# Kernel optimization log

Hardware: AMD Instinct MI355X
Metric: run time of the kernel (lower is better)

## Reference

```python
import jax, jax.numpy as jnp
import numpy as np
from jax import lax

HEAD = 8; DIM = 16; R = 3; R_T = 2
K_AREA = (2 * R + 1) ** 2   # 49 window positions
NT = 2 * R_T + 1            # 5 time taps
POSENC_SCALE = 10; N_FREQ = 10  # enc_dims=64 -> 64//(2*3)=10 freqs per axis


def conv3d(x, w, b):
    y = lax.conv_general_dilated(x, w, (1, 1, 1), 'SAME',
                                 dimension_numbers=('NCDHW', 'OIDHW', 'NCDHW'))
    return y + b[None, :, None, None, None]


def make_coord2(h, w):
    # LIIF-style pixel-center coords in [-1,1], channel order (y, x)
    ys = -1.0 + (2.0 * jnp.arange(h) + 1.0) / h
    xs = -1.0 + (2.0 * jnp.arange(w) + 1.0) / w
    yy, xx = jnp.meshgrid(ys, xs, indexing='ij')
    return jnp.stack([yy, xx], -1)


def gather2d_nearest(img, coord_yx):
    # img (B,C,H,W); coord (B,Q,K,2) normalized (y,x); grid_sample nearest, align_corners=False, zero pad
    B, C, H, W = img.shape
    iy = jnp.round(((coord_yx[..., 0] + 1.0) * H - 1.0) / 2.0)
    ix = jnp.round(((coord_yx[..., 1] + 1.0) * W - 1.0) / 2.0)
    valid = (iy >= 0) & (iy < H) & (ix >= 0) & (ix < W)
    idx = (jnp.clip(iy, 0, H - 1) * W + jnp.clip(ix, 0, W - 1)).astype(jnp.int32)
    flat = idx.reshape(B, -1)
    out = jnp.take_along_axis(img.reshape(B, C, H * W), flat[:, None, :], axis=2)
    out = out.reshape(B, C, *idx.shape[1:]) * valid[:, None].astype(img.dtype)
    return out  # (B,C,Q,K)


def trilinear(vol, coord_tyx):
    # vol (B,C,D,H,W); coord (B,Q,3) normalized (t,y,x); grid_sample bilinear 3D, align_corners=False, zero pad
    B, C, D, H, W = vol.shape
    iz = ((coord_tyx[..., 0] + 1.0) * D - 1.0) / 2.0
    iy = ((coord_tyx[..., 1] + 1.0) * H - 1.0) / 2.0
    ix = ((coord_tyx[..., 2] + 1.0) * W - 1.0) / 2.0
    z0 = jnp.floor(iz); y0 = jnp.floor(iy); x0 = jnp.floor(ix)
    wz = iz - z0; wy = iy - y0; wx = ix - x0
    volf = vol.reshape(B, C, D * H * W)

    def corner(zc, yc, xc, w):
        valid = (zc >= 0) & (zc < D) & (yc >= 0) & (yc < H) & (xc >= 0) & (xc < W)
        idx = (jnp.clip(zc, 0, D - 1) * (H * W) + jnp.clip(yc, 0, H - 1) * W
               + jnp.clip(xc, 0, W - 1)).astype(jnp.int32)
        v = jnp.take_along_axis(volf, idx[:, None, :], axis=2)  # (B,C,Q)
        return v * (w * valid.astype(vol.dtype))[:, None, :]

    out = 0.0
    for dz in (0, 1):
        for dy in (0, 1):
            for dx in (0, 1):
                w = ((wz if dz else 1 - wz) * (wy if dy else 1 - wy)
                     * (wx if dx else 1 - wx))
                out = out + corner(z0 + dz, y0 + dy, x0 + dx, w)
    return out  # (B,C,Q)


def forward(feat_img, scale, times, W_ch, b_ch, W_q, b_q, W_k, b_k, W_v, b_v,
            B_pe, W_pb, b_pb, W1, b1, W2, b2, W3, b3, W4, b4, W5, b5):
    feat = conv3d(feat_img, W_ch, b_ch)
    bs, fc, ft, fh, fw = feat.shape
    times_np = np.asarray(times).reshape(-1) * (ft - 1)
    Hh, Wh = fh * scale, fw * scale
    hr = make_coord2(Hh, Wh).reshape(1, -1, 2).astype(feat.dtype)
    hr = jnp.broadcast_to(hr, (bs, Hh * Wh, 2))  # (B,Q,2)
    q = hr.shape[1]
    # nearest LR pixel-center coords (grid_sample nearest over coord map)
    iy = jnp.clip(jnp.round(((hr[..., 0] + 1) * fh - 1) / 2), 0, fh - 1)
    ix = jnp.clip(jnp.round(((hr[..., 1] + 1) * fw - 1) / 2), 0, fw - 1)
    center = jnp.stack([-1 + (2 * iy + 1) / fh, -1 + (2 * ix + 1) / fw], -1)[:, :, None, :]
    dh = jnp.linspace(-R, R, 2 * R + 1) * (2.0 / fh)
    dw = jnp.linspace(-R, R, 2 * R + 1) * (2.0 / fw)
    gy, gx = jnp.meshgrid(dh, dw, indexing='ij')
    delta = jnp.stack([gy, gx], -1).reshape(1, 1, -1, 2)
    samp_k = center + delta  # (B,Q,K,2) key sampling coords
    feat_q = conv3d(feat, W_q, b_q)
    feat_k = conv3d(feat, W_k, b_k)
    feat_v = conv3d(feat, W_v, b_v)
    rel_cell = jnp.full((bs, q, 2), 2.0 / scale, feat.dtype)
    rel0 = hr[:, :, None, :] - samp_k  # (B,Q,K,2)
    dhd = DIM // HEAD
    preds = []
    for t in times_np:
        ct = int(round(float(t)))
        rel_time = (float(t) - ct) * 2.0 / NT
        idxs = np.clip(ct + np.arange(-R_T, R_T + 1), 0, ft - 1)
        fq_w = feat_q[:, :, idxs]
        fk_w = feat_k[:, :, idxs]
        fv_w = feat_v[:, :, idxs]
        coord3d = jnp.concatenate([jnp.full_like(hr[..., :1], rel_time), hr], -1)
        sq = trilinear(fq_w, coord3d)  # (B,C,Q)
        qh = sq.transpose(0, 2, 1).reshape(bs, q, HEAD, dhd)
        feats = []
        for dt in range(NT):
            tc = rel_time - (dt - R_T) * 2.0 / NT
            rel = jnp.concatenate([jnp.full_like(rel0[..., :1], tc), rel0], -1)
            rel = rel * jnp.asarray([NT, fh, fw], rel.dtype)
            proj = rel @ B_pe.T  # (B,Q,K,3*N_FREQ)
            enc = jnp.concatenate([jnp.sin(proj), jnp.cos(proj)], -1)
            pb = enc @ W_pb + b_pb  # (B,Q,K,HEAD), gamma=1
            kf = gather2d_nearest(fk_w[:, :, dt], samp_k).transpose(0, 2, 3, 1)
            kf = kf.reshape(bs, q, K_AREA, HEAD, dhd)
            scores = jnp.einsum('bqhd,bqkhd->bqkh', qh, kf) / np.sqrt(dhd).astype(np.float32)
            attn = jax.nn.softmax(scores + pb, axis=2)  # softmax over window
            vf = gather2d_nearest(fv_w[:, :, dt], samp_k).transpose(0, 2, 3, 1)
            vf = vf.reshape(bs, q, K_AREA, HEAD, dhd)
            feats.append((vf * attn[..., None]).reshape(bs, q, -1))
        feat_in = jnp.concatenate(feats, -1)           # (B,Q,DIM*K_AREA*NT)
        feat_back = sq.transpose(0, 2, 1)              # (B,Q,DIM)
        feat_in = jnp.concatenate([feat_in, feat_back, rel_cell], -1)
        h = jax.nn.gelu(feat_in @ W1 + b1, approximate=False)
        h = jax.nn.gelu(h @ W2 + b2, approximate=False)
        h = jax.nn.gelu(h @ W3 + b3, approximate=False)
        h = jax.nn.gelu(h @ W4 + b4, approximate=False)
        pred = (h @ W5 + b5).transpose(0, 2, 1).reshape(bs, 3, Hh, Wh)
        preds.append(pred)
    return jnp.stack(preds, 0)  # (n_times, B, 3, Hh, Wh)


def setup_inputs() -> dict:
    key = jax.random.key(0)
    ks = jax.random.split(key, 24)
    bs, in_dim, T, fh, fw = 1, 64, 6, 32, 32
    dim, head = 16, 8
    mlp_in = dim * K_AREA * NT + dim + 2  # 3938

    def w(k, shape, s=0.02):
        return jax.random.normal(k, shape, jnp.float32) * s

    freqs = 2.0 ** np.linspace(0, POSENC_SCALE, N_FREQ)
    B_pe = np.zeros((3 * N_FREQ, 3), np.float32)
    for a in range(3):
        B_pe[a * N_FREQ:(a + 1) * N_FREQ, a] = freqs
    return {
        'feat_img': jax.random.normal(ks[0], (bs, in_dim, T, fh, fw), jnp.float32),
        'scale': 4,
        'times': jax.random.uniform(ks[1], (1,), jnp.float32),
        'W_ch': w(ks[2], (dim, in_dim, 3, 3, 3)), 'b_ch': w(ks[3], (dim,)),
        'W_q': w(ks[4], (dim, dim, 3, 3, 3)), 'b_q': w(ks[5], (dim,)),
        'W_k': w(ks[6], (dim, dim, 3, 3, 3)), 'b_k': w(ks[7], (dim,)),
        'W_v': w(ks[8], (dim, dim, 3, 3, 3)), 'b_v': w(ks[9], (dim,)),
        'B_pe': jnp.asarray(B_pe),
        'W_pb': w(ks[10], (2 * 3 * N_FREQ, head)), 'b_pb': w(ks[11], (head,)),
        'W1': w(ks[12], (mlp_in, 256)), 'b1': w(ks[13], (256,)),
        'W2': w(ks[14], (256, 256)), 'b2': w(ks[15], (256,)),
        'W3': w(ks[16], (256, 256)), 'b3': w(ks[17], (256,)),
        'W4': w(ks[18], (256, 256)), 'b4': w(ks[19], (256,)),
        'W5': w(ks[20], (256, 3)), 'b5': w(ks[21], (3,)),
    }


def reference(feat_img, scale, times, W_ch, b_ch, W_q, b_q, W_k, b_k, W_v, b_v,
              B_pe, W_pb, b_pb, W1, b1, W2, b2, W3, b3, W4, b4, W5, b5):
    return forward(feat_img, scale, times, W_ch, b_ch, W_q, b_q, W_k, b_k, W_v, b_v,
                   B_pe, W_pb, b_pb, W1, b1, W2, b2, W3, b3, W4, b4, W5, b5)
```

## Files before the change

kernel.cpp:

```cpp
#include <hip/hip_runtime.h>

typedef __attribute__((ext_vector_type(8))) short bf16x8;
typedef __attribute__((ext_vector_type(8))) unsigned short u16x8;
typedef __attribute__((ext_vector_type(4))) float f32x4;

#define WSB_FEAT 0u
#define WSB_FQ   393216u
#define WSB_FK   786432u
#define WSB_FV   1179648u
#define WSB_META 1572864u
#define WSB_HA0  1574912u
#define WSB_HA1  18352128u
#define WSB_W1H  35129344u
#define WSB_W234 39258112u
#define WSB_FEAT1 39651328u

#define NH 256

__device__ __forceinline__ float gelu_f(float x) {
  return 0.5f * x * (1.0f + erff(x * 0.70710678118654752f));
}
__device__ __forceinline__ unsigned short f2bf(float x) {
  unsigned int u = __float_as_uint(x);
  u += 0x7fffu + ((u >> 16) & 1u);
  return (unsigned short)(u >> 16);
}
__device__ __forceinline__ float bf2f(unsigned short h) {
  return __uint_as_float(((unsigned int)h) << 16);
}
__device__ __forceinline__ void split2(float a, unsigned short& hi, unsigned short& lo) {
  hi = f2bf(a);
  lo = f2bf(a - bf2f(hi));
}
__device__ __forceinline__ unsigned int cvt_pk_bf16(float a, float b) {
  unsigned int r;
  asm("v_cvt_pk_bf16_f32 %0, %1, %2" : "=v"(r) : "v"(a), "v"(b));
  return r;
}

__global__ __launch_bounds__(512) void pre_kernel(
    const float* __restrict__ in, const float* __restrict__ W,
    const float* __restrict__ times, const float* __restrict__ Bpe,
    const float* __restrict__ Wpb, const float* __restrict__ bpb,
    const float* __restrict__ W1, const float* __restrict__ W2,
    const float* __restrict__ W3, const float* __restrict__ W4,
    float* __restrict__ feat0, float* __restrict__ feat1,
    float* __restrict__ meta,
    unsigned short* __restrict__ W1h, unsigned short* __restrict__ W234h) {
  __shared__ float win[4896];
  const int tid = threadIdx.x;
  if (blockIdx.x < 384) {
    const int half = blockIdx.x / 192;
    const int sp = blockIdx.x - half*192;
    const int t = sp >> 5, y = sp & 31;
    const int x = tid & 31, cop = tid >> 5;
    float acc = 0.f;
    const int cbase = half*32;
    for (int ci0 = cbase; ci0 < cbase + 32; ci0 += 16) {
      __syncthreads();
      for (int e = tid; e < 4896; e += 512) {
        int ci = e / 306, rem = e - ci*306;
        int tz = rem / 102, rem2 = rem - tz*102;
        int dy = rem2 / 34, xx = rem2 - dy*34;
        int gt = t + tz - 1, gy = y + dy - 1, gx = xx - 1;
        float v = 0.f;
        if (gt >= 0 && gt < 6 && gy >= 0 && gy < 32 && gx >= 0 && gx < 32)
          v = in[((ci0 + ci)*6 + gt)*1024 + gy*32 + gx];
        win[e] = v;
      }
      __syncthreads();
      for (int ci = 0; ci < 16; ++ci) {
        const float* w0 = W + (cop*64 + ci0 + ci)*27;
        const float* wr = win + ci*306;
        #pragma unroll
        for (int tz = 0; tz < 3; ++tz)
          #pragma unroll
          for (int dy = 0; dy < 3; ++dy)
            #pragma unroll
            for (int dx = 0; dx < 3; ++dx)
              acc += wr[(tz*3 + dy)*34 + x + dx] * w0[(tz*3 + dy)*3 + dx];
      }
    }
    float* dst = half ? feat1 : feat0;
    dst[(t*1024 + y*32 + x)*16 + cop] = acc;
  } else if (blockIdx.x == 384) {
    const float t5f = times[0] * 5.0f;
    const double ct_d = rint((double)t5f);
    const int ct = (int)ct_d;
    const double rt = ((double)t5f - ct_d) * 2.0 / 5.0;
    const float rtf = (float)rt;
    if (tid == 0) {
      float iz = ((rtf + 1.0f)*5.0f - 1.0f) / 2.0f;
      float z0 = floorf(iz);
      meta[0] = iz - z0;
      meta[1] = z0;
      for (int d = 0; d < 5; ++d) {
        int ix = ct + d - 2; ix = ix < 0 ? 0 : (ix > 5 ? 5 : ix);
        meta[2 + d] = (float)ix;
      }
    }
    if (tid < 40) {
      int dt = tid >> 3, h = tid & 7;
      double tcd = rt - (double)(dt - 2) * 2.0 / 5.0;
      float rs = (float)tcd * 5.0f;
      float acc = bpb[h];
      for (int j = 0; j < 10; ++j) {
        float pr = rs * Bpe[j*3 + 0];
        acc += sinf(pr) * Wpb[j*8 + h] + cosf(pr) * Wpb[(30+j)*8 + h];
      }
      meta[16 + tid] = acc;
    }
    if (tid < 224) {
      int p = tid / 56, ky = (tid >> 3) % 7, h = tid & 7;
      float r = (float)(2*p - 3) * 0.25f - 2.0f * (float)(ky - 3);
      float accy = 0.f, accx = 0.f;
      for (int j = 0; j < 10; ++j) {
        float pry = r * Bpe[(10+j)*3 + 1];
        accy += sinf(pry) * Wpb[(10+j)*8 + h] + cosf(pry) * Wpb[(40+j)*8 + h];
        float prx = r * Bpe[(20+j)*3 + 2];
        accx += sinf(prx) * Wpb[(20+j)*8 + h] + cosf(prx) * Wpb[(50+j)*8 + h];
      }
      meta[64 + tid]  = accy;
      meta[288 + tid] = accx;
    }
  } else if (tid < 256) {
    const int rblk = blockIdx.x - 385;
    const int n = tid;
    unsigned short tmp[32];
    if (rblk < 126) {
      const int s = rblk;
      #pragma unroll
      for (int j = 0; j < 32; ++j) {
        int p = s*32 + j;
        float w = 0.f;
        if (p < 4000) {
          int dt = p / 800, r = p - dt*800;
          if (r < 784) w = W1[(dt*784 + r)*256 + n];
        } else {
          int j2 = p - 4000;
          if (j2 < 18) w = W1[(3920 + j2)*256 + n];
        }
        tmp[j] = f2bf(w);
      }
      unsigned short* dh = W1h + ((size_t)(s*256 + n))*32;
      #pragma unroll
      for (int v = 0; v < 4; ++v) {
        u16x8 xv;
        #pragma unroll
        for (int j = 0; j < 8; ++j) xv[j] = tmp[v*8 + j];
        *(u16x8*)(dh + v*8) = xv;
      }
    } else {
      const int blk = rblk - 126;
      const int m = blk >> 3, s = blk & 7;
      const float* Wm = (m == 0) ? W2 : ((m == 1) ? W3 : W4);
      #pragma unroll
      for (int j = 0; j < 32; ++j) tmp[j] = f2bf(Wm[(s*32 + j)*256 + n]);
      unsigned short* dh = W234h + (size_t)m*65536 + ((size_t)(s*256 + n))*32;
      #pragma unroll
      for (int v = 0; v < 4; ++v) {
        u16x8 xv;
        #pragma unroll
        for (int j = 0; j < 8; ++j) xv[j] = tmp[v*8 + j];
        *(u16x8*)(dh + v*8) = xv;
      }
    }
  }
}

__global__ __launch_bounds__(512) void conv_qkv_kernel(
    const float* __restrict__ f0, const float* __restrict__ f1,
    const float* __restrict__ bch,
    const float* __restrict__ Wq, const float* __restrict__ bq,
    const float* __restrict__ Wk, const float* __restrict__ bk,
    const float* __restrict__ Wv, const float* __restrict__ bv,
    float* __restrict__ fq, float* __restrict__ fk, float* __restrict__ fv) {
  __shared__ float win[4896];
  __shared__ float sbch[16];
  const int blk = blockIdx.x;
  const int m = blk / 192;
  const int sp = blk - m*192;
  const int t = sp >> 5, y = sp & 31;
  const int tid = threadIdx.x;
  const int x = tid & 31, cop = tid >> 5;
  if (tid < 16) sbch[tid] = bch[tid];
  __syncthreads();
  for (int e = tid; e < 4896; e += 512) {
    int tz = e / 1632, rem = e - tz*1632;
    int dy = rem / 544, rem2 = rem - dy*544;
    int ci = rem2 / 34, xx = rem2 - ci*34;
    int gt = t + tz - 1, gy = y + dy - 1, gx = xx - 1;
    float v = 0.f;
    if (gt >= 0 && gt < 6 && gy >= 0 && gy < 32 && gx >= 0 && gx < 32) {
      const int idx = ((gt*32 + gy)*32 + gx)*16 + ci;
      v = f0[idx] + f1[idx] + sbch[ci];
    }
    win[e] = v;
  }
  __syncthreads();
  const float* Wm = (m == 0) ? Wq : ((m == 1) ? Wk : Wv);
  const float* bm = (m == 0) ? bq : ((m == 1) ? bk : bv);
  float*       fm = (m == 0) ? fq : ((m == 1) ? fk : fv);
  float a0 = 0.f, a1 = 0.f;
  for (int ci = 0; ci < 16; ci += 2) {
    const float* w0 = Wm + (cop*16 + ci)*27;
    #pragma unroll
    for (int tz = 0; tz < 3; ++tz)
      #pragma unroll
      for (int dy = 0; dy < 3; ++dy) {
        const float* wr0 = win + ((tz*3 + dy)*16 + ci)*34 + x;
        #pragma unroll
        for (int dx = 0; dx < 3; ++dx) {
          const int tap = (tz*3 + dy)*3 + dx;
          a0 += wr0[dx]      * w0[tap];
          a1 += wr0[34 + dx] * w0[27 + tap];
        }
      }
  }
  fm[(t*1024 + y*32 + x)*16 + cop] = a0 + a1 + bm[cop];
}

template<int CHL, int CHH>
__device__ __forceinline__ void attn_dt(
    int dt, int cj0, int ci0, int tid,
    int q, int h, int ay, int ax, int py, int px,
    int goct, int qr, int nb0,
    const float* __restrict__ fk, const float* __restrict__ fv,
    const unsigned short* __restrict__ W1h,
    const float* sPt, const float* sPy, const float* sPx, const float* sMeta,
    const float* sQh, float* sK, float* sV,
    unsigned short* sA0, unsigned short* sA1,
    f32x4 (&acc)[4][2]) {
  __syncthreads();
  const int tg = (int)sMeta[2 + dt];
  for (int e = tid; e < 2048; e += 512) {
    const int sel = e >> 10, r = e & 1023;
    const int wy8 = r >> 7, wx8 = (r >> 4) & 7, c = r & 15;
    const int gy = cj0 + wy8 - 3, gx = ci0 + wx8 - 3;
    float v = 0.f;
    if (gy >= 0 && gy < 32 && gx >= 0 && gx < 32)
      v = (sel ? fv : fk)[((tg*32 + gy)*32 + gx)*16 + c];
    (sel ? sV : sK)[r] = v;
  }
  __syncthreads();

  const float qv0 = sQh[q*16 + 2*h], qv1 = sQh[q*16 + 2*h + 1];
  const float ptv = sPt[dt*8 + h];
  float ev[49];
  float ssum = 0.f;
  #pragma unroll
  for (int ky = 0; ky < 7; ++ky) {
    const float basey = ptv + sPy[(py*7 + ky)*8 + h];
    #pragma unroll
    for (int kx = 0; kx < 7; ++kx) {
      const float2 kv = *(const float2*)&sK[((ay + ky)*8 + ax + kx)*16 + 2*h];
      const float sc = (qv0*kv.x + qv1*kv.y) * 0.70710678118654752f + basey + sPx[(px*7 + kx)*8 + h];
      const float x = __expf(sc);
      ev[ky*7 + kx] = x;
      ssum += x;
    }
  }
  const float dinv = 1.f / ssum;

#define FILL_CHUNK(CH, BUF) do {                                            \
    _Pragma("unroll")                                                       \
    for (int kk = 0; kk < 10; ++kk) {                                       \
      const int k = (CH)*10 + kk;                                           \
      float a0 = 0.f, a1 = 0.f;                                             \
      if (k < 49) {                                                         \
        const int ky = k / 7, kx = k - ky*7;                                \
        const float e2 = ev[k] * dinv;                                      \
        const float2 vv = *(const float2*)&sV[((ay + ky)*8 + ax + kx)*16 + 2*h]; \
        a0 = e2 * vv.x; a1 = e2 * vv.y;                                     \
      }                                                                     \
      const int off = ((((kk >> 1)*4 + (kk & 1)*2 + (h >> 2))*4 + (q >> 4))*16 + (q & 15))*8 + 2*(h & 3); \
      *(unsigned int*)&(BUF)[off] = cvt_pk_bf16(a0, a1);                    \
    } } while (0)

  FILL_CHUNK(CHL, sA0);
  __syncthreads();
  #pragma unroll
  for (int ch = CHL; ch <= CHH; ++ch) {
    unsigned short* bufR = ((ch - CHL) & 1) ? sA1 : sA0;
    unsigned short* bufW = ((ch - CHL) & 1) ? sA0 : sA1;
    #pragma unroll
    for (int sc2 = 0; sc2 < 5; ++sc2) {
      const int s_g = dt*25 + ch*5 + sc2;
      const unsigned short* bh_p = W1h + (size_t)(s_g*256 + nb0 + qr)*32 + goct*8;
      const bf16x8 bh0 = *(const bf16x8*)bh_p;
      const bf16x8 bh1 = *(const bf16x8*)(bh_p + 512);
      #pragma unroll
      for (int mt = 0; mt < 4; ++mt) {
        const int aoff = (((sc2*4 + goct)*4 + mt)*16 + qr)*8;
        const bf16x8 ah = *(const bf16x8*)&bufR[aoff];
        acc[mt][0] = __builtin_amdgcn_mfma_f32_16x16x32_bf16(ah, bh0, acc[mt][0], 0, 0, 0);
        acc[mt][1] = __builtin_amdgcn_mfma_f32_16x16x32_bf16(ah, bh1, acc[mt][1], 0, 0, 0);
      }
    }
    if (ch < CHH) FILL_CHUNK(ch + 1, bufW);
    __syncthreads();
  }
#undef FILL_CHUNK
}

__global__ __launch_bounds__(512, 4) void attn_l1_kernel(
    const float* __restrict__ fq, const float* __restrict__ fk,
    const float* __restrict__ fv, const float* __restrict__ meta,
    const unsigned short* __restrict__ W1h,
    float* __restrict__ hA0, float* __restrict__ hA1) {
  __shared__ float sPt[40], sPy[224], sPx[224], sMeta[8];
  __shared__ float sQh[1024];
  __shared__ float sK[1024], sV[1024];
  __shared__ __align__(16) unsigned short sA0[10240];
  __shared__ __align__(16) unsigned short sA1[10240];

  const int tid = threadIdx.x;
  const int cp = blockIdx.x >> 1, bh = blockIdx.x & 1;
  const int cj0 = (cp >> 4) * 2, ci0 = (cp & 15) * 2;

  if (tid < 8) sMeta[tid] = meta[tid];
  if (tid < 40) sPt[tid] = meta[16 + tid];
  if (tid < 224) { sPy[tid] = meta[64 + tid]; sPx[tid] = meta[288 + tid]; }
  __syncthreads();
  const float wz = sMeta[0];
  const int z0 = (int)sMeta[1];
  const int tgz0 = (int)sMeta[2 + z0];
  const int tgz1 = (int)sMeta[3 + z0];

  for (int e = tid; e < 1024; e += 512) {
    const int q = e >> 4, c = e & 15;
    const int pyp = q >> 3, pxp = q & 7;
    const int cj = cj0 + (pyp >> 2), ci = ci0 + (pxp >> 2);
    const int py = pyp & 3, px = pxp & 3;
    const int y0 = cj + ((py < 2) ? -1 : 0);
    const int x0 = ci + ((px < 2) ? -1 : 0);
    const float wy = (py == 0) ? 0.625f : (py == 1) ? 0.875f : (py == 2) ? 0.125f : 0.375f;
    const float wx = (px == 0) ? 0.625f : (px == 1) ? 0.875f : (px == 2) ? 0.125f : 0.375f;
    float s = 0.f;
    #pragma unroll
    for (int dz = 0; dz < 2; ++dz) {
      const int tg = dz ? tgz1 : tgz0;
      const float wzz = dz ? wz : (1.f - wz);
      #pragma unroll
      for (int dy = 0; dy < 2; ++dy) {
        const int yy = y0 + dy;
        const float wyy = dy ? wy : (1.f - wy);
        if (yy < 0 || yy > 31) continue;
        #pragma unroll
        for (int dx = 0; dx < 2; ++dx) {
          const int xx = x0 + dx;
          const float wxx = dx ? wx : (1.f - wx);
          if (xx < 0 || xx > 31) continue;
          s += ((wzz * wyy) * wxx) * fq[((tg*32 + yy)*32 + xx)*16 + c];
        }
      }
    }
    sQh[e] = s;
  }

  f32x4 acc[4][2];
  #pragma unroll
  for (int a = 0; a < 4; ++a) {
    acc[a][0] = (f32x4){0.f, 0.f, 0.f, 0.f};
    acc[a][1] = (f32x4){0.f, 0.f, 0.f, 0.f};
  }

  const int lane = tid & 63, wid = tid >> 6;
  const int goct = lane >> 4, qr = lane & 15;
  const int nb0 = wid * 32;
  const int q = tid >> 3, h = tid & 7;
  const int ay = q >> 5, ax = (q >> 2) & 1;
  const int py = (q >> 3) & 3, px = q & 3;

  if (!bh) {
    attn_dt<0,4>(0, cj0, ci0, tid, q, h, ay, ax, py, px, goct, qr, nb0,
                 fk, fv, W1h, sPt, sPy, sPx, sMeta, sQh, sK, sV, sA0, sA1, acc);
    attn_dt<0,4>(1, cj0, ci0, tid, q, h, ay, ax, py, px, goct, qr, nb0,
                 fk, fv, W1h, sPt, sPy, sPx, sMeta, sQh, sK, sV, sA0, sA1, acc);
    attn_dt<0,1>(2, cj0, ci0, tid, q, h, ay, ax, py, px, goct, qr, nb0,
                 fk, fv, W1h, sPt, sPy, sPx, sMeta, sQh, sK, sV, sA0, sA1, acc);
    __syncthreads();
    for (int e = tid; e < 2048; e += 512) {
      const int q2 = e >> 5, r2 = e & 31;
      const float a = (r2 < 16) ? sQh[q2*16 + r2] : ((r2 < 18) ? 0.5f : 0.f);
      const int off = ((((r2 >> 3))*4 + (q2 >> 4))*16 + (q2 & 15))*8 + (r2 & 7);
      sA0[off] = f2bf(a);
    }
    __syncthreads();
    const unsigned short* bh_p = W1h + (size_t)(125*256 + nb0 + qr)*32 + goct*8;
    const bf16x8 bh0 = *(const bf16x8*)bh_p;
    const bf16x8 bh1 = *(const bf16x8*)(bh_p + 512);
    #pragma unroll
    for (int mt = 0; mt < 4; ++mt) {
      const int aoff = ((goct*4 + mt)*16 + qr)*8;
      const bf16x8 ah = *(const bf16x8*)&sA0[aoff];
      acc[mt][0] = __builtin_amdgcn_mfma_f32_16x16x32_bf16(ah, bh0, acc[mt][0], 0, 0, 0);
      acc[mt][1] = __builtin_amdgcn_mfma_f32_16x16x32_bf16(ah, bh1, acc[mt][1], 0, 0, 0);
    }
  } else {
    attn_dt<2,4>(2, cj0, ci0, tid, q, h, ay, ax, py, px, goct, qr, nb0,
                 fk, fv, W1h, sPt, sPy, sPx, sMeta, sQh, sK, sV, sA0, sA1, acc);
    attn_dt<0,4>(3, cj0, ci0, tid, q, h, ay, ax, py, px, goct, qr, nb0,
                 fk, fv, W1h, sPt, sPy, sPx, sMeta, sQh, sK, sV, sA0, sA1, acc);
    attn_dt<0,4>(4, cj0, ci0, tid, q, h, ay, ax, py, px, goct, qr, nb0,
                 fk, fv, W1h, sPt, sPy, sPx, sMeta, sQh, sK, sV, sA0, sA1, acc);
  }

  float* hp = bh ? hA1 : hA0;
  #pragma unroll
  for (int nt = 0; nt < 2; ++nt) {
    const int n = nb0 + nt*16 + qr;
    #pragma unroll
    for (int mt = 0; mt < 4; ++mt) {
      #pragma unroll
      for (int r = 0; r < 4; ++r) {
        const int ql = mt*16 + goct*4 + r;
        const int row = (cj0*4 + (ql >> 3))*128 + ci0*4 + (ql & 7);
        hp[row*NH + n] = acc[mt][nt][r];
      }
    }
  }
}

__global__ __launch_bounds__(512) void mlp234o_kernel(
    const float* __restrict__ hA0, const float* __restrict__ hA1,
    const unsigned short* __restrict__ W234h, const float* __restrict__ b1,
    const float* __restrict__ b2, const float* __restrict__ b3,
    const float* __restrict__ b4, const float* __restrict__ W5,
    const float* __restrict__ b5, float* __restrict__ out) {
  __shared__ __align__(16) unsigned short aH[8192];
  __shared__ __align__(16) unsigned short aL[8192];
  __shared__ float sW5[768];
  __shared__ float sB5[3];

  const int tid = threadIdx.x, lane = tid & 63, wid = tid >> 6;
  const int goct = lane >> 4, qr = lane & 15, nb0 = wid * 32;
  const int qbase = blockIdx.x * 32;

  for (int e = tid; e < 768; e += 512) sW5[e] = W5[e];
  if (tid < 3) sB5[tid] = b5[tid];

  {
    #pragma unroll
    for (int u = 0; u < 2; ++u) {
      const int idx = tid*2 + u;
      const int q0_ = idx >> 5, rem = idx & 31;
      const int s0_ = rem >> 2, g = rem & 3;
      const size_t off = (size_t)(qbase + q0_)*NH + s0_*32 + g*8;
      const float4 pa0 = *(const float4*)(hA0 + off);
      const float4 pa1 = *(const float4*)(hA0 + off + 4);
      const float4 pb0 = *(const float4*)(hA1 + off);
      const float4 pb1 = *(const float4*)(hA1 + off + 4);
      const float4 bb0 = *(const float4*)(b1 + s0_*32 + g*8);
      const float4 bb1 = *(const float4*)(b1 + s0_*32 + g*8 + 4);
      float vals[8] = {pa0.x + pb0.x + bb0.x, pa0.y + pb0.y + bb0.y,
                       pa0.z + pb0.z + bb0.z, pa0.w + pb0.w + bb0.w,
                       pa1.x + pb1.x + bb1.x, pa1.y + pb1.y + bb1.y,
                       pa1.z + pb1.z + bb1.z, pa1.w + pb1.w + bb1.w};
      bf16x8 hiv, lov;
      #pragma unroll
      for (int j = 0; j < 8; ++j) {
        const float v = gelu_f(vals[j]);
        unsigned short h_, l_;
        split2(v, h_, l_);
        hiv[j] = (short)h_; lov[j] = (short)l_;
      }
      const int ao = (((s0_*4 + g)*2 + (q0_ >> 4))*16 + (q0_ & 15))*8;
      *(bf16x8*)&aH[ao] = hiv;
      *(bf16x8*)&aL[ao] = lov;
    }
  }

  for (int layer = 0; layer < 3; ++layer) {
    const unsigned short* Wh = W234h + (size_t)layer*65536;
    const float* bptr = (layer == 0) ? b2 : ((layer == 1) ? b3 : b4);
    __syncthreads();
    f32x4 acc[2][2];
    #pragma unroll
    for (int a = 0; a < 2; ++a) {
      acc[a][0] = (f32x4){0.f, 0.f, 0.f, 0.f};
      acc[a][1] = (f32x4){0.f, 0.f, 0.f, 0.f};
    }
    #pragma unroll
    for (int s = 0; s < 8; ++s) {
      const unsigned short* bh_p = Wh + (size_t)(s*256 + nb0 + qr)*32 + goct*8;
      const bf16x8 bh0 = *(const bf16x8*)bh_p;
      const bf16x8 bh1 = *(const bf16x8*)(bh_p + 512);
      #pragma unroll
      for (int mt = 0; mt < 2; ++mt) {
        const int aoff = (((s*4 + goct)*2 + mt)*16 + qr)*8;
        const bf16x8 ah = *(const bf16x8*)&aH[aoff];
        const bf16x8 al = *(const bf16x8*)&aL[aoff];
        acc[mt][0] = __builtin_amdgcn_mfma_f32_16x16x32_bf16(ah, bh0, acc[mt][0], 0, 0, 0);
        acc[mt][0] = __builtin_amdgcn_mfma_f32_16x16x32_bf16(al, bh0, acc[mt][0], 0, 0, 0);
        acc[mt][1] = __builtin_amdgcn_mfma_f32_16x16x32_bf16(ah, bh1, acc[mt][1], 0, 0, 0);
        acc[mt][1] = __builtin_amdgcn_mfma_f32_16x16x32_bf16(al, bh1, acc[mt][1], 0, 0, 0);
      }
    }
    __syncthreads();
    #pragma unroll
    for (int nt = 0; nt < 2; ++nt) {
      const int n = nb0 + nt*16 + qr;
      const float bb = bptr[n];
      #pragma unroll
      for (int mt = 0; mt < 2; ++mt) {
        #pragma unroll
        for (int r = 0; r < 4; ++r) {
          const int qq = mt*16 + goct*4 + r;
          const float v = gelu_f(acc[mt][nt][r] + bb);
          unsigned short h_, l_; split2(v, h_, l_);
          const int ao = ((((n >> 5)*4 + ((n >> 3) & 3))*2 + mt)*16 + (qq & 15))*8 + (n & 7);
          aH[ao] = h_; aL[ao] = l_;
        }
      }
    }
  }
  __syncthreads();
  if (tid < 96) {
    const int c = tid >> 5, qq = tid & 31;
    const int mt = qq >> 4, qrr = qq & 15;
    float a = sB5[c];
    #pragma unroll 4
    for (int k8 = 0; k8 < 32; ++k8) {
      const int ao = ((k8*2 + mt)*16 + qrr)*8;
      const bf16x8 hv = *(const bf16x8*)&aH[ao];
      const bf16x8 lv = *(const bf16x8*)&aL[ao];
      #pragma unroll
      for (int j = 0; j < 8; ++j)
        a += (bf2f((unsigned short)hv[j]) + bf2f((unsigned short)lv[j])) * sW5[(k8*8 + j)*3 + c];
    }
    out[c*16384 + qbase + qq] = a;
  }
}

extern "C" void kernel_launch(void* const* d_in, const int* in_sizes, int n_in,
                              void* d_out, int out_size, void* d_ws, size_t ws_size,
                              hipStream_t stream) {
  const float* feat_img = (const float*)d_in[0];
  const float* times    = (const float*)d_in[2];
  const float* W_ch     = (const float*)d_in[3];
  const float* b_ch     = (const float*)d_in[4];
  const float* W_q      = (const float*)d_in[5];
  const float* b_q      = (const float*)d_in[6];
  const float* W_k      = (const float*)d_in[7];
  const float* b_k      = (const float*)d_in[8];
  const float* W_v      = (const float*)d_in[9];
  const float* b_v      = (const float*)d_in[10];
  const float* B_pe     = (const float*)d_in[11];
  const float* W_pb     = (const float*)d_in[12];
  const float* b_pb     = (const float*)d_in[13];
  const float* W1       = (const float*)d_in[14];
  const float* b1       = (const float*)d_in[15];
  const float* W2       = (const float*)d_in[16];
  const float* b2       = (const float*)d_in[17];
  const float* W3       = (const float*)d_in[18];
  const float* b3       = (const float*)d_in[19];
  const float* W4       = (const float*)d_in[20];
  const float* b4       = (const float*)d_in[21];
  const float* W5       = (const float*)d_in[22];
  const float* b5       = (const float*)d_in[23];

  char* wsb = (char*)d_ws;
  float* feat0 = (float*)(wsb + WSB_FEAT);
  float* feat1 = (float*)(wsb + WSB_FEAT1);
  float* fq   = (float*)(wsb + WSB_FQ);
  float* fk   = (float*)(wsb + WSB_FK);
  float* fv   = (float*)(wsb + WSB_FV);
  float* meta = (float*)(wsb + WSB_META);
  float* hA0  = (float*)(wsb + WSB_HA0);
  float* hA1  = (float*)(wsb + WSB_HA1);
  unsigned short* W1h   = (unsigned short*)(wsb + WSB_W1H);
  unsigned short* W234h = (unsigned short*)(wsb + WSB_W234);

  pre_kernel<<<535, 512, 0, stream>>>(feat_img, W_ch, times, B_pe, W_pb, b_pb,
                                      W1, W2, W3, W4, feat0, feat1, meta, W1h, W234h);
  conv_qkv_kernel<<<576, 512, 0, stream>>>(feat0, feat1, b_ch,
                                           W_q, b_q, W_k, b_k, W_v, b_v, fq, fk, fv);
  attn_l1_kernel<<<512, 512, 0, stream>>>(fq, fk, fv, meta, W1h, hA0, hA1);
  mlp234o_kernel<<<512, 512, 0, stream>>>(hA0, hA1, W234h, b1, b2, b3, b4, W5, b5, (float*)d_out);
}
```

Measured before the change: 152.7 us.

## Prefetch next time-tap K/V window into registers and raise MFMA wave priority

The K/V window gather for the next time tap is now issued into registers right after the softmax of the current tap. Its global-load latency can then hide behind the FILL/MFMA chunk loop instead of stalling at the start of each tap. The MFMA inner loop is also bracketed with s_setprio to favour matrix issue over the fill phase of other waves. This adds four live registers per thread and leaves the priority effect uncertain under the 512-thread, 4-block launch bounds.

```diff
diff --git a/kernel.cpp b/kernel.cpp
--- a/kernel.cpp
+++ b/kernel.cpp
@@ -220,27 +220,41 @@
   fm[(t*1024 + y*32 + x)*16 + cop] = a0 + a1 + bm[cop];
 }
 
-template<int CHL, int CHH>
+__device__ __forceinline__ void load_kv_regs(
+    int tg, int cj0, int ci0, int tid,
+    const float* __restrict__ fk, const float* __restrict__ fv,
+    float (&kvr)[4]) {
+  #pragma unroll
+  for (int u = 0; u < 4; ++u) {
+    const int e = tid + u*512;
+    const int sel = e >> 10, r = e & 1023;
+    const int wy8 = r >> 7, wx8 = (r >> 4) & 7, c = r & 15;
+    const int gy = cj0 + wy8 - 3, gx = ci0 + wx8 - 3;
+    float v = 0.f;
+    if (gy >= 0 && gy < 32 && gx >= 0 && gx < 32)
+      v = (sel ? fv : fk)[((tg*32 + gy)*32 + gx)*16 + c];
+    kvr[u] = v;
+  }
+}
+
+template<int CHL, int CHH, bool PRE>
 __device__ __forceinline__ void attn_dt(
     int dt, int cj0, int ci0, int tid,
     int q, int h, int ay, int ax, int py, int px,
     int goct, int qr, int nb0,
     const float* __restrict__ fk, const float* __restrict__ fv,
     const unsigned short* __restrict__ W1h,
-    const float* sPt, const float* sPy, const float* sPx, const float* sMeta,
+    const float* sPt, const float* sPy, const float* sPx,
     const float* sQh, float* sK, float* sV,
     unsigned short* sA0, unsigned short* sA1,
+    float (&kvr)[4], int tg_next,
     f32x4 (&acc)[4][2]) {
   __syncthreads();
-  const int tg = (int)sMeta[2 + dt];
-  for (int e = tid; e < 2048; e += 512) {
+  #pragma unroll
+  for (int u = 0; u < 4; ++u) {
+    const int e = tid + u*512;
     const int sel = e >> 10, r = e & 1023;
-    const int wy8 = r >> 7, wx8 = (r >> 4) & 7, c = r & 15;
-    const int gy = cj0 + wy8 - 3, gx = ci0 + wx8 - 3;
-    float v = 0.f;
-    if (gy >= 0 && gy < 32 && gx >= 0 && gx < 32)
-      v = (sel ? fv : fk)[((tg*32 + gy)*32 + gx)*16 + c];
-    (sel ? sV : sK)[r] = v;
+    (sel ? sV : sK)[r] = kvr[u];
   }
   __syncthreads();
 
@@ -261,6 +275,8 @@
     }
   }
   const float dinv = 1.f / ssum;
+
+  if (PRE) load_kv_regs(tg_next, cj0, ci0, tid, fk, fv, kvr);
 
 #define FILL_CHUNK(CH, BUF) do {                                            \
     _Pragma("unroll")                                                       \
@@ -283,6 +299,7 @@
   for (int ch = CHL; ch <= CHH; ++ch) {
     unsigned short* bufR = ((ch - CHL) & 1) ? sA1 : sA0;
     unsigned short* bufW = ((ch - CHL) & 1) ? sA0 : sA1;
+    __builtin_amdgcn_s_setprio(1);
     #pragma unroll
     for (int sc2 = 0; sc2 < 5; ++sc2) {
       const int s_g = dt*25 + ch*5 + sc2;
@@ -297,6 +314,7 @@
         acc[mt][1] = __builtin_amdgcn_mfma_f32_16x16x32_bf16(ah, bh1, acc[mt][1], 0, 0, 0);
       }
     }
+    __builtin_amdgcn_s_setprio(0);
     if (ch < CHH) FILL_CHUNK(ch + 1, bufW);
     __syncthreads();
   }
@@ -326,6 +344,7 @@
   const int z0 = (int)sMeta[1];
   const int tgz0 = (int)sMeta[2 + z0];
   const int tgz1 = (int)sMeta[3 + z0];
+  const int tgd[5] = {(int)sMeta[2], (int)sMeta[3], (int)sMeta[4], (int)sMeta[5], (int)sMeta[6]};
 
   for (int e = tid; e < 1024; e += 512) {
     const int q = e >> 4, c = e & 15;
@@ -372,13 +391,15 @@
   const int ay = q >> 5, ax = (q >> 2) & 1;
   const int py = (q >> 3) & 3, px = q & 3;
 
+  float kvr[4];
   if (!bh) {
-    attn_dt<0,4>(0, cj0, ci0, tid, q, h, ay, ax, py, px, goct, qr, nb0,
-                 fk, fv, W1h, sPt, sPy, sPx, sMeta, sQh, sK, sV, sA0, sA1, acc);
-    attn_dt<0,4>(1, cj0, ci0, tid, q, h, ay, ax, py, px, goct, qr, nb0,
-                 fk, fv, W1h, sPt, sPy, sPx, sMeta, sQh, sK, sV, sA0, sA1, acc);
-    attn_dt<0,1>(2, cj0, ci0, tid, q, h, ay, ax, py, px, goct, qr, nb0,
-                 fk, fv, W1h, sPt, sPy, sPx, sMeta, sQh, sK, sV, sA0, sA1, acc);
+    load_kv_regs(tgd[0], cj0, ci0, tid, fk, fv, kvr);
+    attn_dt<0,4,true >(0, cj0, ci0, tid, q, h, ay, ax, py, px, goct, qr, nb0,
+                       fk, fv, W1h, sPt, sPy, sPx, sQh, sK, sV, sA0, sA1, kvr, tgd[1], acc);
+    attn_dt<0,4,true >(1, cj0, ci0, tid, q, h, ay, ax, py, px, goct, qr, nb0,
+                       fk, fv, W1h, sPt, sPy, sPx, sQh, sK, sV, sA0, sA1, kvr, tgd[2], acc);
+    attn_dt<0,1,false>(2, cj0, ci0, tid, q, h, ay, ax, py, px, goct, qr, nb0,
+                       fk, fv, W1h, sPt, sPy, sPx, sQh, sK, sV, sA0, sA1, kvr, 0, acc);
     __syncthreads();
     for (int e = tid; e < 2048; e += 512) {
       const int q2 = e >> 5, r2 = e & 31;
@@ -398,12 +419,13 @@
       acc[mt][1] = __builtin_amdgcn_mfma_f32_16x16x32_bf16(ah, bh1, acc[mt][1], 0, 0, 0);
     }
   } else {
-    attn_dt<2,4>(2, cj0, ci0, tid, q, h, ay, ax, py, px, goct, qr, nb0,
-                 fk, fv, W1h, sPt, sPy, sPx, sMeta, sQh, sK, sV, sA0, sA1, acc);
-    attn_dt<0,4>(3, cj0, ci0, tid, q, h, ay, ax, py, px, goct, qr, nb0,
-                 fk, fv, W1h, sPt, sPy, sPx, sMeta, sQh, sK, sV, sA0, sA1, acc);
-    attn_dt<0,4>(4, cj0, ci0, tid, q, h, ay, ax, py, px, goct, qr, nb0,
-                 fk, fv, W1h, sPt, sPy, sPx, sMeta, sQh, sK, sV, sA0, sA1, acc);
+    load_kv_regs(tgd[2], cj0, ci0, tid, fk, fv, kvr);
+    attn_dt<2,4,true >(2, cj0, ci0, tid, q, h, ay, ax, py, px, goct, qr, nb0,
+                       fk, fv, W1h, sPt, sPy, sPx, sQh, sK, sV, sA0, sA1, kvr, tgd[3], acc);
+    attn_dt<0,4,true >(3, cj0, ci0, tid, q, h, ay, ax, py, px, goct, qr, nb0,
+                       fk, fv, W1h, sPt, sPy, sPx, sQh, sK, sV, sA0, sA1, kvr, tgd[4], acc);
+    attn_dt<0,4,false>(4, cj0, ci0, tid, q, h, ay, ax, py, px, goct, qr, nb0,
+                       fk, fv, W1h, sPt, sPy, sPx, sQh, sK, sV, sA0, sA1, kvr, 0, acc);
   }
 
   float* hp = bh ? hA1 : hA0;
```

Result: slower. 169.0 us (+10.7%).
